# Optimization experiments

Measured on AMD Instinct MI355X. Metric: run time of the kernel, lower is better.

Reference implementation:

```python
import jax, jax.numpy as jnp
import numpy as np

N, DIN, DOUT, R, E = 100000, 128, 256, 4, 600000
EPS = 1e-12


def setup_inputs() -> dict:
    key = jax.random.key(0)
    ks = jax.random.split(key, 8)
    x = jax.random.normal(ks[0], (N, DIN), dtype=jnp.float32)
    edge_index = jax.random.randint(ks[1], (R, 2, E), 0, N, dtype=jnp.int32)
    s1 = 1.0 / np.sqrt(DIN)
    s2 = 1.0 / np.sqrt(DOUT)
    W1n = jax.random.uniform(ks[2], (R, DOUT, DIN), jnp.float32, -s1, s1)
    W1r = jax.random.uniform(ks[3], (R, DOUT, DIN), jnp.float32, -s1, s1)
    b1 = jnp.zeros((R, DOUT), jnp.float32)
    W2n = jax.random.uniform(ks[4], (R, DOUT, DOUT), jnp.float32, -s2, s2)
    W2r = jax.random.uniform(ks[5], (R, DOUT, DOUT), jnp.float32, -s2, s2)
    b2 = jnp.zeros((R, DOUT), jnp.float32)
    return {"x": x, "edge_index": edge_index, "W1n": W1n, "b1": b1,
            "W1r": W1r, "W2n": W2n, "b2": b2, "W2r": W2r}


def _hetero_sage_layer(x, edge_index, Wn, b, Wr):
    # per-relation sum-aggregate of source features into destinations: [R, N, D]
    agg = jax.vmap(
        lambda e: jax.ops.segment_sum(x[e[0]], e[1], num_segments=N)
    )(edge_index)
    # SAGEConv: lin_l(agg) + bias + lin_r(x); mean across relations (to_hetero aggr='mean')
    out = (jnp.einsum('rnd,rod->rno', agg, Wn)
           + b[:, None, :]
           + jnp.einsum('nd,rod->rno', x, Wr))
    return out.mean(axis=0)  # [N, DOUT]


def _l2_normalize(h):
    nrm = jnp.sqrt(jnp.sum(h * h, axis=-1, keepdims=True))
    return h / jnp.maximum(nrm, EPS)


def reference(x, edge_index, W1n, b1, W1r, W2n, b2, W2r):
    h = _hetero_sage_layer(x, edge_index, W1n, b1, W1r)
    h = jax.nn.relu(_l2_normalize(h))  # dropout is identity in eval mode
    out = _hetero_sage_layer(h, edge_index, W2n, b2, W2r)
    return out  # x_dict['note']
```

## Files before the change

kernel.cpp:

```cpp
#include <hip/hip_runtime.h>
#include <hip/hip_bf16.h>

#define NN 100000
#define DIN 128
#define DOUT 256
#define RR 4
#define EE 600000
#define NB (RR * NN)
#define SCAN_BLKS 400
#define SCAN_CHUNK 1000

typedef __attribute__((ext_vector_type(4))) float f32x4;
typedef __attribute__((ext_vector_type(8))) short short8;
typedef __attribute__((ext_vector_type(2))) uint uint2v;

__device__ __forceinline__ float bf2f(ushort u) {
    union { unsigned int i; float f; } v; v.i = ((unsigned int)u) << 16; return v.f;
}
__device__ __forceinline__ ushort f2bf(float f) {
    union { float f; unsigned int i; } v; v.f = f;
    unsigned int r = v.i + 0x7fff + ((v.i >> 16) & 1);
    return (ushort)(r >> 16);
}

__device__ __forceinline__ void ld_g2l16(const void* g, void* l) {
    __builtin_amdgcn_global_load_lds(
        (const __attribute__((address_space(1))) void*)g,
        (__attribute__((address_space(3))) void*)l, 16, 0, 0);
}

__device__ __forceinline__ void store_w(ushort* W, int kd, int o, float s) {
    int cs = ((kd >> 3) & 7) ^ (o & 7);
    W[((size_t)(kd >> 6) * 256 + o) * 64 + cs * 8 + (kd & 7)] = f2bf(s);
}

#define W1ELEMS (5 * 128 * 256)
#define W2ELEMS (5 * 256 * 256)
__global__ void wprep_all(const float* __restrict__ W1n, const float* __restrict__ W1r,
                          const float* __restrict__ W2n, const float* __restrict__ W2r,
                          const float* __restrict__ b1, const float* __restrict__ b2,
                          ushort* __restrict__ W1c, ushort* __restrict__ W2c,
                          float* __restrict__ b1s, float* __restrict__ b2s) {
    int idx = blockIdx.x * blockDim.x + threadIdx.x;
    if (idx < W1ELEMS) {
        int p = idx / (128 * 256), rem = idx - p * (128 * 256);
        int k = rem >> 8, o = rem & 255;
        float s;
        if (p == 0) {
            s = 0.f;
            for (int r = 0; r < RR; ++r) s += W1r[(size_t)r * DOUT * DIN + (long)o * DIN + k];
        } else {
            s = W1n[(size_t)(p - 1) * DOUT * DIN + (long)o * DIN + k];
        }
        store_w(W1c, p * 128 + k, o, s * 0.25f);
        return;
    }
    idx -= W1ELEMS;
    if (idx < W2ELEMS) {
        int p = idx / (256 * 256), rem = idx - p * (256 * 256);
        int k = rem >> 8, o = rem & 255;
        float s;
        if (p == 0) {
            s = 0.f;
            for (int r = 0; r < RR; ++r) s += W2r[(size_t)r * DOUT * DOUT + (long)o * DOUT + k];
        } else {
            s = W2n[(size_t)(p - 1) * DOUT * DOUT + (long)o * DOUT + k];
        }
        store_w(W2c, p * 256 + k, o, s * 0.25f);
        return;
    }
    idx -= W2ELEMS;
    if (idx < 512) {
        int o = idx & 255;
        const float* b = (idx < 256) ? b1 : b2;
        float s = 0.f;
        for (int r = 0; r < RR; ++r) s += b[(long)r * 256 + o];
        ((idx < 256) ? b1s : b2s)[o] = s * 0.25f;
    }
}

__global__ void deg_count(const int* __restrict__ ei, int* __restrict__ deg) {
    int idx = blockIdx.x * blockDim.x + threadIdx.x;
    if (idx >= RR * (EE / 4)) return;
    int r = idx / (EE / 4), j = idx - r * (EE / 4);
    int4 d = ((const int4*)(ei + (size_t)r * 2 * EE + EE))[j];
    atomicAdd(&deg[r * NN + d.x], 1);
    atomicAdd(&deg[r * NN + d.y], 1);
    atomicAdd(&deg[r * NN + d.z], 1);
    atomicAdd(&deg[r * NN + d.w], 1);
}

__global__ __launch_bounds__(256) void scan_part(const int* __restrict__ deg,
                                                 int* __restrict__ bsum) {
    int b = blockIdx.x, t = threadIdx.x;
    int s = 0;
    for (int i = t; i < SCAN_CHUNK; i += 256) s += deg[b * SCAN_CHUNK + i];
    for (int o = 32; o > 0; o >>= 1) s += __shfl_down(s, o);
    __shared__ int red[4];
    if ((t & 63) == 0) red[t >> 6] = s;
    __syncthreads();
    if (t == 0) bsum[b] = red[0] + red[1] + red[2] + red[3];
}

__global__ __launch_bounds__(512) void scan_top(int* __restrict__ bsum) {
    __shared__ int v[512];
    int t = threadIdx.x;
    v[t] = (t < SCAN_BLKS) ? bsum[t] : 0;
    __syncthreads();
    for (int st = 1; st < 512; st <<= 1) {
        int tmp = (t >= st) ? v[t - st] : 0;
        __syncthreads();
        v[t] += tmp;
        __syncthreads();
    }
    if (t < SCAN_BLKS) bsum[t] = (t == 0) ? 0 : v[t - 1];
}

__global__ __launch_bounds__(256) void scan_final(int* __restrict__ degc,
                                                  const int* __restrict__ bsum,
                                                  int* __restrict__ off) {
    __shared__ int lv[1024];
    __shared__ int ts[256];
    int b = blockIdx.x, t = threadIdx.x;
    for (int i = t; i < 1024; i += 256)
        lv[i] = (i < SCAN_CHUNK) ? degc[b * SCAN_CHUNK + i] : 0;
    __syncthreads();
    int i0 = t * 4;
    int v0 = lv[i0], v1 = lv[i0 + 1], v2 = lv[i0 + 2], v3 = lv[i0 + 3];
    ts[t] = v0 + v1 + v2 + v3;
    __syncthreads();
    for (int st = 1; st < 256; st <<= 1) {
        int tmp = (t >= st) ? ts[t - st] : 0;
        __syncthreads();
        ts[t] += tmp;
        __syncthreads();
    }
    int run = bsum[b] + (t ? ts[t - 1] : 0);
    if (i0 < SCAN_CHUNK) {
        int base = b * SCAN_CHUNK + i0;
        off[base + 0] = run; degc[base + 0] = run; run += v0;
        off[base + 1] = run; degc[base + 1] = run; run += v1;
        off[base + 2] = run; degc[base + 2] = run; run += v2;
        off[base + 3] = run; degc[base + 3] = run; run += v3;
    }
    if (b == SCAN_BLKS - 1 && t == 255) off[NB] = bsum[b] + ts[255];
}

__global__ void fill_csr(const int* __restrict__ ei, int* __restrict__ cursor,
                         int* __restrict__ elist) {
    int idx = blockIdx.x * blockDim.x + threadIdx.x;
    if (idx >= RR * (EE / 4)) return;
    int r = idx / (EE / 4), j = idx - r * (EE / 4);
    int4 s = ((const int4*)(ei + (size_t)r * 2 * EE))[j];
    int4 d = ((const int4*)(ei + (size_t)r * 2 * EE + EE))[j];
    elist[atomicAdd(&cursor[r * NN + d.x], 1)] = s.x;
    elist[atomicAdd(&cursor[r * NN + d.y], 1)] = s.y;
    elist[atomicAdd(&cursor[r * NN + d.z], 1)] = s.z;
    elist[atomicAdd(&cursor[r * NN + d.w], 1)] = s.w;
}

__global__ void cvt_x(const float* __restrict__ x, ushort* __restrict__ XB) {
    int t = blockIdx.x * blockDim.x + threadIdx.x;
    if (t >= NN * 32) return;
    int n = t >> 5, c4 = (t & 31) * 4;
    float4 v = *(const float4*)&x[(size_t)n * 128 + c4];
    ushort4 o = {f2bf(v.x), f2bf(v.y), f2bf(v.z), f2bf(v.w)};
    *(ushort4*)&XB[(size_t)n * 128 + c4] = o;
}

template <int D>
__global__ void gather_bf16(const ushort* __restrict__ feat,
                            const int* __restrict__ elist, const int* __restrict__ off,
                            ushort* __restrict__ agg, int sout, int chunk) {
    constexpr int V = D / 64;
    int wv = blockIdx.x * 4 + (threadIdx.x >> 6);
    int lane = threadIdx.x & 63;
    if (wv >= NN * chunk) return;
    int n = wv / chunk, rl = wv - n * chunk;
    int b = rl * NN + n;
    int beg = __builtin_amdgcn_readfirstlane(off[b]);
    int end = __builtin_amdgcn_readfirstlane(off[b + 1]);
    float acc[V];
#pragma unroll
    for (int v = 0; v < V; ++v) acc[v] = 0.f;
    const ushort* fbase = feat + lane * V;
    int e = beg;
    for (; e + 4 <= end; e += 4) {
        int s0 = elist[e], s1 = elist[e + 1], s2 = elist[e + 2], s3 = elist[e + 3];
        if constexpr (V == 2) {
            ushort2 a0 = *(const ushort2*)(fbase + (size_t)s0 * D);
            ushort2 a1 = *(const ushort2*)(fbase + (size_t)s1 * D);
            ushort2 a2 = *(const ushort2*)(fbase + (size_t)s2 * D);
            ushort2 a3 = *(const ushort2*)(fbase + (size_t)s3 * D);
            acc[0] += (bf2f(a0.x) + bf2f(a1.x)) + (bf2f(a2.x) + bf2f(a3.x));
            acc[1] += (bf2f(a0.y) + bf2f(a1.y)) + (bf2f(a2.y) + bf2f(a3.y));
        } else {
            ushort4 a0 = *(const ushort4*)(fbase + (size_t)s0 * D);
            ushort4 a1 = *(const ushort4*)(fbase + (size_t)s1 * D);
            ushort4 a2 = *(const ushort4*)(fbase + (size_t)s2 * D);
            ushort4 a3 = *(const ushort4*)(fbase + (size_t)s3 * D);
            acc[0] += (bf2f(a0.x) + bf2f(a1.x)) + (bf2f(a2.x) + bf2f(a3.x));
            acc[1] += (bf2f(a0.y) + bf2f(a1.y)) + (bf2f(a2.y) + bf2f(a3.y));
            acc[2] += (bf2f(a0.z) + bf2f(a1.z)) + (bf2f(a2.z) + bf2f(a3.z));
            acc[3] += (bf2f(a0.w) + bf2f(a1.w)) + (bf2f(a2.w) + bf2f(a3.w));
        }
    }
    for (; e < end; ++e) {
        int s0 = elist[e];
        if constexpr (V == 2) {
            ushort2 a = *(const ushort2*)(fbase + (size_t)s0 * D);
            acc[0] += bf2f(a.x); acc[1] += bf2f(a.y);
        } else {
            ushort4 a = *(const ushort4*)(fbase + (size_t)s0 * D);
            acc[0] += bf2f(a.x); acc[1] += bf2f(a.y);
            acc[2] += bf2f(a.z); acc[3] += bf2f(a.w);
        }
    }
    ushort* op = agg + (size_t)n * sout + rl * D + lane * V;
    if constexpr (V == 2) {
        uint u = (uint)f2bf(acc[0]) | ((uint)f2bf(acc[1]) << 16);
        *(uint*)op = u;
    } else {
        uint2v u;
        u.x = (uint)f2bf(acc[0]) | ((uint)f2bf(acc[1]) << 16);
        u.y = (uint)f2bf(acc[2]) | ((uint)f2bf(acc[3]) << 16);
        *(uint2v*)op = u;
    }
}

template <int MODE>
__global__ __launch_bounds__(256, 2) void gemm_fused(
    const ushort* __restrict__ F, int ldf, int K1,
    const ushort* __restrict__ G, int ldg, int K2,
    const ushort* __restrict__ W, const float* __restrict__ bias,
    void* __restrict__ Cout, int M) {
    __shared__ ushort lA[128 * 64];
    __shared__ ushort lB[256 * 64];
    const int tid = threadIdx.x;
    const int w = tid >> 6, lane = tid & 63;
    const int row0 = blockIdx.x * 128;

    f32x4 acc[8][4];
#pragma unroll
    for (int i = 0; i < 8; ++i)
#pragma unroll
        for (int j = 0; j < 4; ++j) acc[i][j] = {0.f, 0.f, 0.f, 0.f};

    const int arow = lane >> 3;
    const int asrc = ((lane & 7) ^ arow) << 3;
    const int ldst = lane * 8;
    const ushort* aF[4]; const ushort* aG[4];
#pragma unroll
    for (int c = 0; c < 4; ++c) {
        int rg = row0 + w * 32 + c * 8 + arow;
        if (rg > M - 1) rg = M - 1;
        aF[c] = F + (size_t)rg * ldf + asrc;
        aG[c] = G + (size_t)rg * ldg + asrc;
    }
    const int nt = (K1 + K2) >> 6;

    for (int t = 0; t < nt; ++t) {
        __syncthreads();
        int kb = t << 6;
#pragma unroll
        for (int c = 0; c < 4; ++c) {
            const ushort* src = (kb < K1) ? (aF[c] + kb) : (aG[c] + (kb - K1));
            ld_g2l16(src, &lA[(w * 32 + c * 8) * 64 + ldst]);
        }
        const ushort* wb = W + (size_t)t * (256 * 64);
#pragma unroll
        for (int c = 0; c < 8; ++c)
            ld_g2l16(wb + (w * 64 + c * 8) * 64 + ldst, &lB[(w * 64 + c * 8) * 64 + ldst]);
        asm volatile("s_waitcnt vmcnt(0)" ::: "memory");
        __syncthreads();
        __builtin_amdgcn_s_setprio(1);
#pragma unroll
        for (int ks = 0; ks < 2; ++ks) {
            const int co = (((ks * 4 + (lane >> 4)) ^ (lane & 7)) << 3);
            short8 af[8];
#pragma unroll
            for (int rf = 0; rf < 8; ++rf)
                af[rf] = *(const short8*)&lA[(rf * 16 + (lane & 15)) * 64 + co];
#pragma unroll
            for (int cf = 0; cf < 4; ++cf) {
                short8 bf8 = *(const short8*)&lB[(w * 64 + cf * 16 + (lane & 15)) * 64 + co];
#pragma unroll
                for (int rf = 0; rf < 8; ++rf)
                    acc[rf][cf] = __builtin_amdgcn_mfma_f32_16x16x32_bf16(
                        af[rf], bf8, acc[rf][cf], 0, 0, 0);
            }
        }
        __builtin_amdgcn_s_setprio(0);
    }

#pragma unroll
    for (int cf = 0; cf < 4; ++cf) {
        float badd = bias[w * 64 + cf * 16 + (lane & 15)];
#pragma unroll
        for (int rf = 0; rf < 8; ++rf)
#pragma unroll
            for (int m = 0; m < 4; ++m) acc[rf][cf][m] += badd;
    }

    if constexpr (MODE == 0) {
        float* Cf = (float*)Cout;
#pragma unroll
        for (int cf = 0; cf < 4; ++cf) {
            int col = w * 64 + cf * 16 + (lane & 15);
#pragma unroll
            for (int rf = 0; rf < 8; ++rf)
#pragma unroll
                for (int m = 0; m < 4; ++m) {
                    int r = row0 + rf * 16 + (lane >> 4) * 4 + m;
                    if (r < M)
                        __builtin_nontemporal_store(acc[rf][cf][m],
                                                    &Cf[(size_t)r * 256 + col]);
                }
        }
    } else {
        float* rs = (float*)lA;
        float ss[8][4];
#pragma unroll
        for (int rf = 0; rf < 8; ++rf)
#pragma unroll
            for (int m = 0; m < 4; ++m) {
                float s = 0.f;
#pragma unroll
                for (int cf = 0; cf < 4; ++cf) s += acc[rf][cf][m] * acc[rf][cf][m];
#pragma unroll
                for (int o = 1; o < 16; o <<= 1) s += __shfl_xor(s, o);
                ss[rf][m] = s;
            }
        __syncthreads();
        if ((lane & 15) == 0) {
#pragma unroll
            for (int rf = 0; rf < 8; ++rf)
#pragma unroll
                for (int m = 0; m < 4; ++m)
                    rs[w * 128 + rf * 16 + (lane >> 4) * 4 + m] = ss[rf][m];
        }
        __syncthreads();
        uint* HBw = (uint*)Cout;
#pragma unroll
        for (int rf = 0; rf < 8; ++rf)
#pragma unroll
            for (int m = 0; m < 4; ++m) {
                int tr = rf * 16 + (lane >> 4) * 4 + m;
                float tot = rs[tr] + rs[128 + tr] + rs[256 + tr] + rs[384 + tr];
                float inv = 1.0f / fmaxf(sqrtf(tot), 1e-12f);
                int r = row0 + tr;
#pragma unroll
                for (int cf = 0; cf < 4; ++cf) {
                    float v = fmaxf(acc[rf][cf][m] * inv, 0.f);
                    uint u = f2bf(v);
                    uint pu = __shfl_xor(u, 1);
                    if (!(lane & 1) && r < M)
                        HBw[(size_t)r * 128 + ((w * 64 + cf * 16 + (lane & 15)) >> 1)] =
                            u | (pu << 16);
                }
            }
    }
}

extern "C" void kernel_launch(void* const* d_in, const int* in_sizes, int n_in,
                              void* d_out, int out_size, void* d_ws, size_t ws_size,
                              hipStream_t stream) {
    const float* x   = (const float*)d_in[0];
    const int*   ei  = (const int*)d_in[1];
    const float* W1n = (const float*)d_in[2];
    const float* b1  = (const float*)d_in[3];
    const float* W1r = (const float*)d_in[4];
    const float* W2n = (const float*)d_in[5];
    const float* b2  = (const float*)d_in[6];
    const float* W2r = (const float*)d_in[7];

    ushort* HB  = (ushort*)d_ws;
    ushort* G1  = HB + (size_t)NN * 256;
    ushort* G2  = G1 + (size_t)NN * 512;
    ushort* XB  = G2;
    int* elist  = (int*)(G2 + (size_t)NN * 1024);
    int* degc   = elist + (size_t)RR * EE;
    int* off    = degc + NB;
    int* bsum   = off + NB + 1;
    ushort* W1c = (ushort*)(bsum + 512);
    ushort* W2c = W1c + 640 * 256;
    float* b1s  = (float*)(W2c + 1280 * 256);
    float* b2s  = b1s + 256;

    hipMemsetAsync(degc, 0, (size_t)NB * sizeof(int), stream);
    deg_count<<<(RR * (EE / 4) + 255) / 256, 256, 0, stream>>>(ei, degc);
    scan_part<<<SCAN_BLKS, 256, 0, stream>>>(degc, bsum);
    scan_top<<<1, 512, 0, stream>>>(bsum);
    scan_final<<<SCAN_BLKS, 256, 0, stream>>>(degc, bsum, off);
    fill_csr<<<(RR * (EE / 4) + 255) / 256, 256, 0, stream>>>(ei, degc, elist);

    {
        int total = W1ELEMS + W2ELEMS + 512;
        wprep_all<<<(total + 255) / 256, 256, 0, stream>>>(W1n, W1r, W2n, W2r, b1, b2,
                                                           W1c, W2c, b1s, b2s);
    }
    cvt_x<<<(NN * 32 + 255) / 256, 256, 0, stream>>>(x, XB);

    const int ggrid = (NN + 127) / 128;

    gather_bf16<128><<<NN, 256, 0, stream>>>(XB, elist, off, G1, 512, RR);
    gemm_fused<1><<<ggrid, 256, 0, stream>>>(XB, 128, 128, G1, 512, 512, W1c, b1s, HB, NN);

    gather_bf16<256><<<NN, 256, 0, stream>>>(HB, elist, off, G2, 1024, RR);
    gemm_fused<0><<<ggrid, 256, 0, stream>>>(HB, 256, 256, G2, 1024, 1024, W2c, b2s,
                                             d_out, NN);
}
```

Measured before the change: 799.6 us.

## Partition degree-count and CSR-fill atomics by destination bits across block groups

deg_count and fill_csr become persistent grid-stride kernels with 2048 blocks. Each block is assigned one of 8 partitions, keyed on bits 8-10 of the destination id, and only performs atomics for edges in its partition. The aim is to localize the atomic traffic on deg/cursor to a region per block group, which may help L2 or XCD locality on MI355X. The cost is that every partition re-reads the whole edge list, eight times the index loads, and adds branch divergence.

```diff
diff --git a/kernel.cpp b/kernel.cpp
--- a/kernel.cpp
+++ b/kernel.cpp
@@ -9,6 +9,7 @@
 #define NB (RR * NN)
 #define SCAN_BLKS 400
 #define SCAN_CHUNK 1000
+#define PBLKS 2048
 
 typedef __attribute__((ext_vector_type(4))) float f32x4;
 typedef __attribute__((ext_vector_type(8))) short short8;
@@ -79,15 +80,36 @@
     }
 }
 
-__global__ void deg_count(const int* __restrict__ ei, int* __restrict__ deg) {
-    int idx = blockIdx.x * blockDim.x + threadIdx.x;
-    if (idx >= RR * (EE / 4)) return;
-    int r = idx / (EE / 4), j = idx - r * (EE / 4);
-    int4 d = ((const int4*)(ei + (size_t)r * 2 * EE + EE))[j];
-    atomicAdd(&deg[r * NN + d.x], 1);
-    atomicAdd(&deg[r * NN + d.y], 1);
-    atomicAdd(&deg[r * NN + d.z], 1);
-    atomicAdd(&deg[r * NN + d.w], 1);
+__global__ __launch_bounds__(256) void deg_count(const int* __restrict__ ei,
+                                                 int* __restrict__ deg) {
+    const int CH = EE / 4;
+    int p = blockIdx.x & 7;
+    const int stride = (PBLKS / 8) * 256;
+    for (int idx = (blockIdx.x >> 3) * 256 + threadIdx.x; idx < RR * CH; idx += stride) {
+        int r = idx / CH, j = idx - r * CH;
+        int4 d = ((const int4*)(ei + (size_t)r * 2 * EE + EE))[j];
+        if (((d.x >> 8) & 7) == p) atomicAdd(&deg[r * NN + d.x], 1);
+        if (((d.y >> 8) & 7) == p) atomicAdd(&deg[r * NN + d.y], 1);
+        if (((d.z >> 8) & 7) == p) atomicAdd(&deg[r * NN + d.z], 1);
+        if (((d.w >> 8) & 7) == p) atomicAdd(&deg[r * NN + d.w], 1);
+    }
+}
+
+__global__ __launch_bounds__(256) void fill_csr(const int* __restrict__ ei,
+                                                int* __restrict__ cursor,
+                                                int* __restrict__ elist) {
+    const int CH = EE / 4;
+    int p = blockIdx.x & 7;
+    const int stride = (PBLKS / 8) * 256;
+    for (int idx = (blockIdx.x >> 3) * 256 + threadIdx.x; idx < RR * CH; idx += stride) {
+        int r = idx / CH, j = idx - r * CH;
+        int4 d = ((const int4*)(ei + (size_t)r * 2 * EE + EE))[j];
+        int4 s = ((const int4*)(ei + (size_t)r * 2 * EE))[j];
+        if (((d.x >> 8) & 7) == p) elist[atomicAdd(&cursor[r * NN + d.x], 1)] = s.x;
+        if (((d.y >> 8) & 7) == p) elist[atomicAdd(&cursor[r * NN + d.y], 1)] = s.y;
+        if (((d.z >> 8) & 7) == p) elist[atomicAdd(&cursor[r * NN + d.z], 1)] = s.z;
+        if (((d.w >> 8) & 7) == p) elist[atomicAdd(&cursor[r * NN + d.w], 1)] = s.w;
+    }
 }
 
 __global__ __launch_bounds__(256) void scan_part(const int* __restrict__ deg,
@@ -144,19 +166,6 @@
         off[base + 3] = run; degc[base + 3] = run; run += v3;
     }
     if (b == SCAN_BLKS - 1 && t == 255) off[NB] = bsum[b] + ts[255];
-}
-
-__global__ void fill_csr(const int* __restrict__ ei, int* __restrict__ cursor,
-                         int* __restrict__ elist) {
-    int idx = blockIdx.x * blockDim.x + threadIdx.x;
-    if (idx >= RR * (EE / 4)) return;
-    int r = idx / (EE / 4), j = idx - r * (EE / 4);
-    int4 s = ((const int4*)(ei + (size_t)r * 2 * EE))[j];
-    int4 d = ((const int4*)(ei + (size_t)r * 2 * EE + EE))[j];
-    elist[atomicAdd(&cursor[r * NN + d.x], 1)] = s.x;
-    elist[atomicAdd(&cursor[r * NN + d.y], 1)] = s.y;
-    elist[atomicAdd(&cursor[r * NN + d.z], 1)] = s.z;
-    elist[atomicAdd(&cursor[r * NN + d.w], 1)] = s.w;
 }
 
 __global__ void cvt_x(const float* __restrict__ x, ushort* __restrict__ XB) {
@@ -388,11 +397,11 @@
     float* b2s  = b1s + 256;
 
     hipMemsetAsync(degc, 0, (size_t)NB * sizeof(int), stream);
-    deg_count<<<(RR * (EE / 4) + 255) / 256, 256, 0, stream>>>(ei, degc);
+    deg_count<<<PBLKS, 256, 0, stream>>>(ei, degc);
     scan_part<<<SCAN_BLKS, 256, 0, stream>>>(degc, bsum);
     scan_top<<<1, 512, 0, stream>>>(bsum);
     scan_final<<<SCAN_BLKS, 256, 0, stream>>>(degc, bsum, off);
-    fill_csr<<<(RR * (EE / 4) + 255) / 256, 256, 0, stream>>>(ei, degc, elist);
+    fill_csr<<<PBLKS, 256, 0, stream>>>(ei, degc, elist);
 
     {
         int total = W1ELEMS + W2ELEMS + 512;
```

After: 718.5 us. -10.1%, faster.
